# Performance work log

Measured on AMD Instinct MI355X. Metric: run time of the kernel, lower is better.

## Reference

```python
import jax, jax.numpy as jnp
import numpy as np

D_MODEL = 1024
N_HEADS = 16
B, T = 2, 2048


def setup_inputs() -> dict:
    key = jax.random.key(0)
    ks = jax.random.split(key, 5)
    scale = 1.0 / np.sqrt(D_MODEL)
    return {
        "x": jax.random.normal(ks[0], (B, T, D_MODEL), dtype=jnp.float32),
        "W_q": jax.random.normal(ks[1], (D_MODEL, D_MODEL), dtype=jnp.float32) * scale,
        "W_k": jax.random.normal(ks[2], (D_MODEL, D_MODEL), dtype=jnp.float32) * scale,
        "W_v": jax.random.normal(ks[3], (D_MODEL, D_MODEL), dtype=jnp.float32) * scale,
        "W_o": jax.random.normal(ks[4], (D_MODEL, D_MODEL), dtype=jnp.float32) * scale,
    }


def reference(x, W_q, W_k, W_v, W_o):
    Bn, Tn, D = x.shape
    H = N_HEADS
    Dh = D // H
    # nn.Linear(x) = x @ W.T ; weights stored as [out, in]
    q = (x @ W_q.T).reshape(Bn, Tn, H, Dh).transpose(0, 2, 1, 3)  # [B,H,T,Dh]
    k = (x @ W_k.T).reshape(Bn, Tn, H, Dh).transpose(0, 2, 1, 3)
    v = (x @ W_v.T).reshape(Bn, Tn, H, Dh).transpose(0, 2, 1, 3)
    scores = jnp.einsum("bhqd,bhkd->bhqk", q, k) / np.sqrt(Dh).astype(np.float32)
    attn = jax.nn.softmax(scores, axis=-1)  # [B,H,T,T]
    out = jnp.einsum("bhqk,bhkd->bhqd", attn, v)  # [B,H,T,Dh]
    out = out.transpose(0, 2, 1, 3).reshape(Bn, Tn, D)
    return out @ W_o.T
```

## Files before the change

kernel.cpp:

```cpp
#include <hip/hip_runtime.h>
#include <stdint.h>
#include <stddef.h>


typedef __bf16  bf16x8  __attribute__((ext_vector_type(8)));
typedef __bf16  bf16x4  __attribute__((ext_vector_type(4)));
typedef float   floatx4 __attribute__((ext_vector_type(4)));
typedef short   short4v __attribute__((ext_vector_type(4)));

#define DEV static __device__ __forceinline__

DEV void ld_g2l16(const void* g, void* l) {
    __builtin_amdgcn_global_load_lds(
        (__attribute__((address_space(1))) void*)g,
        (__attribute__((address_space(3))) void*)l,
        16, 0, 0);
}

DEV floatx4 mfma16(bf16x4 a, bf16x4 b, floatx4 c) {
#if defined(__HIP_DEVICE_COMPILE__)
    return __builtin_amdgcn_mfma_f32_16x16x16bf16_1k(
        __builtin_bit_cast(short4v, a), __builtin_bit_cast(short4v, b),
        c, 0, 0, 0);
#else
    (void)a; (void)b;
    return c;
#endif
}

#define WK_SCALE 0.18033688011112042f

__global__ __launch_bounds__(256) void cvt_all(
    const float* __restrict__ x,
    const float* __restrict__ wq, const float* __restrict__ wk,
    const float* __restrict__ wv, const float* __restrict__ wo,
    __bf16* __restrict__ xb,
    __bf16* __restrict__ wqb, __bf16* __restrict__ wkb,
    __bf16* __restrict__ wvb, __bf16* __restrict__ wob)
{
    unsigned u = blockIdx.x * 256u + threadIdx.x;
    const float* src;
    __bf16* dst;
    unsigned off;
    float mul = 1.0f;
    if (u < 1048576u) {
        src = x; dst = xb; off = u;
    } else {
        unsigned u2 = u - 1048576u;
        unsigned sel = u2 >> 18;
        off = u2 & 0x3FFFFu;
        src = (sel == 0) ? wq : (sel == 1) ? wk : (sel == 2) ? wv : wo;
        dst = (sel == 0) ? wqb : (sel == 1) ? wkb : (sel == 2) ? wvb : wob;
        if (sel == 1) mul = WK_SCALE;
    }
    float4 f = *(const float4*)(src + (size_t)off * 4);
    bf16x4 o = { (__bf16)(f.x * mul), (__bf16)(f.y * mul),
                 (__bf16)(f.z * mul), (__bf16)(f.w * mul) };
    *(bf16x4*)(dst + (size_t)off * 4) = o;
}

template<int BM, int NMAT, bool OUT_F32, bool TR_V>
__global__ __launch_bounds__(256) void gemm_bt(
    const __bf16* __restrict__ A,
    const __bf16* __restrict__ B0, const __bf16* __restrict__ B1,
    const __bf16* __restrict__ B2,
    void* __restrict__ C0, void* __restrict__ C1, void* __restrict__ C2)
{
    constexpr int Kd = 1024;
    constexpr int N  = 1024;
    constexpr int MI = BM / 32;
    constexpr int NA = BM / 64;
    __shared__ __bf16 As[BM * 32];
    __shared__ __bf16 Bs[128 * 32];

    const int t    = threadIdx.x;
    const int wid  = __builtin_amdgcn_readfirstlane(t >> 6);
    const int lane = t & 63;
    const int quad = lane >> 4;
    const int l15  = lane & 15;

    const int bx  = blockIdx.x;
    const int mat = (NMAT > 1) ? (bx >> 3) : 0;
    const int bn  = (NMAT > 1) ? (bx & 7)  : bx;
    const int bm  = blockIdx.y;
    const __bf16* Bm = (mat == 0) ? B0 : (mat == 1) ? B1 : B2;

    const __bf16* pA[NA];
    const __bf16* pB[2];
#pragma unroll
    for (int i = 0; i < NA; ++i) {
        int c    = i * 256 + t;
        int row  = c >> 2;
        int g    = (c & 3) ^ ((row >> 1) & 3);
        pA[i] = A + (size_t)(bm * BM + row) * Kd + g * 8;
    }
#pragma unroll
    for (int i = 0; i < 2; ++i) {
        int c    = i * 256 + t;
        int row  = c >> 2;
        int g    = (c & 3) ^ ((row >> 1) & 3);
        pB[i] = Bm + (size_t)(bn * 128 + row) * Kd + g * 8;
    }

    const int wm = wid >> 1;
    const int wn = wid & 1;
    const int slotr = quad ^ ((l15 >> 1) & 3);

    floatx4 acc[MI][4];
    const floatx4 z = { 0.f, 0.f, 0.f, 0.f };
#pragma unroll
    for (int i = 0; i < MI; ++i)
#pragma unroll
        for (int j = 0; j < 4; ++j) acc[i][j] = z;

    for (int kb = 0; kb < Kd; kb += 32) {
        __syncthreads();
#pragma unroll
        for (int i = 0; i < NA; ++i)
            ld_g2l16(pA[i] + kb, (char*)As + i * 4096 + wid * 1024);
#pragma unroll
        for (int i = 0; i < 2; ++i)
            ld_g2l16(pB[i] + kb, (char*)Bs + i * 4096 + wid * 1024);
        __syncthreads();

        bf16x8 af[MI], bf[4];
#pragma unroll
        for (int i = 0; i < MI; ++i) {
            int rowA = wm * (BM / 2) + i * 16 + l15;
            af[i] = *(const bf16x8*)&As[rowA * 32 + slotr * 8];
        }
#pragma unroll
        for (int j = 0; j < 4; ++j) {
            int rowB = wn * 64 + j * 16 + l15;
            bf[j] = *(const bf16x8*)&Bs[rowB * 32 + slotr * 8];
        }
#pragma unroll
        for (int i = 0; i < MI; ++i)
#pragma unroll
            for (int j = 0; j < 4; ++j)
                acc[i][j] = __builtin_amdgcn_mfma_f32_16x16x32_bf16(
                    af[i], bf[j], acc[i][j], 0, 0, 0);
    }

    const int row0 = bm * BM + wm * (BM / 2);
    const int col0 = bn * 128 + wn * 64;

    if (TR_V && mat == 2) {
        __bf16* Vt = (__bf16*)C2;
        const int bq    = bm >> 4;
        const int tloc0 = (row0 & 2047) + quad * 4;
#pragma unroll
        for (int i = 0; i < MI; ++i)
#pragma unroll
            for (int j = 0; j < 4; ++j) {
                int col = col0 + j * 16 + l15;
                int hh  = col >> 6, dh = col & 63;
                bf16x4 v = { (__bf16)acc[i][j][0], (__bf16)acc[i][j][1],
                             (__bf16)acc[i][j][2], (__bf16)acc[i][j][3] };
                *(bf16x4*)(Vt + ((size_t)(bq * 16 + hh) * 64 + dh) * 2048
                              + tloc0 + i * 16) = v;
            }
    } else {
        void* Cv = (mat == 0) ? C0 : (mat == 1) ? C1 : C2;
#pragma unroll
        for (int i = 0; i < MI; ++i)
#pragma unroll
            for (int j = 0; j < 4; ++j)
#pragma unroll
                for (int r = 0; r < 4; ++r) {
                    int grow = row0 + i * 16 + quad * 4 + r;
                    int gcol = col0 + j * 16 + l15;
                    if (OUT_F32)
                        ((float*)Cv)[(size_t)grow * N + gcol] = acc[i][j][r];
                    else
                        ((__bf16*)Cv)[(size_t)grow * N + gcol] =
                            (__bf16)acc[i][j][r];
                }
    }
}

__global__ __launch_bounds__(256, 2) void flash_kernel(
    const __bf16* __restrict__ Q, const __bf16* __restrict__ K,
    const __bf16* __restrict__ Vt, __bf16* __restrict__ O)
{
    __shared__ __bf16 Qs[128 * 64];
    __shared__ __bf16 Ks[2][64 * 64];
    __shared__ __bf16 Vs[2][64 * 64];

    const int t    = threadIdx.x;
    const int wid  = __builtin_amdgcn_readfirstlane(t >> 6);
    const int half = wid >> 1;
    const int wsub = wid & 1;
    const int lane = t & 63;
    const int quad = lane >> 4;
    const int l15  = lane & 15;
    const int qt   = blockIdx.x;
    const int bh   = blockIdx.y;
    const int b    = bh >> 4, h = bh & 15;

#pragma unroll
    for (int i = 0; i < 4; ++i) {
        int c = i * 256 + t;
        int row = c >> 3;
        int g   = (c & 7) ^ (row & 7);
        ld_g2l16(Q + (size_t)(b * 2048 + qt * 128 + row) * 1024 + h * 64 + g * 8,
                 (char*)Qs + i * 4096 + wid * 1024);
    }

    const __bf16* pK[2];
    const __bf16* pV[2];
#pragma unroll
    for (int i = 0; i < 2; ++i) {
        int c = i * 256 + t;
        int srow = c >> 3;
        int sg   = (c & 7) ^ (srow & 7);
        pK[i] = K  + (size_t)(b * 2048 + srow) * 1024 + h * 64 + sg * 8;
        pV[i] = Vt + (size_t)(bh * 64 + srow) * 2048 + sg * 8;
    }

    __syncthreads();

    bf16x8 qf[4][2];
#pragma unroll
    for (int nb = 0; nb < 4; ++nb)
#pragma unroll
        for (int ks = 0; ks < 2; ++ks) {
            int row  = wsub * 64 + nb * 16 + l15;
            int slot = (ks * 4 + quad) ^ (row & 7);
            qf[nb][ks] = *(const bf16x8*)&Qs[row * 64 + slot * 8];
        }

    int koff[2];
#pragma unroll
    for (int ks = 0; ks < 2; ++ks)
        koff[ks] = l15 * 128 + (((ks * 4 + quad) ^ (l15 & 7)) << 4);
    int voff[4];
#pragma unroll
    for (int k16 = 0; k16 < 4; ++k16)
        voff[k16] = l15 * 128 + (((k16 * 2 + (quad >> 1)) ^ (l15 & 7)) << 4)
                  + (quad & 1) * 8;

    const floatx4 z = { 0.f, 0.f, 0.f, 0.f };
    floatx4 o[4][4];
#pragma unroll
    for (int nb = 0; nb < 4; ++nb)
#pragma unroll
        for (int nd = 0; nd < 4; ++nd) o[nb][nd] = z;
    float lsum[4] = { 0.f, 0.f, 0.f, 0.f };

    for (int it = 0; it < 16; ++it) {
        __syncthreads();
#pragma unroll
        for (int i = 0; i < 2; ++i) {
            ld_g2l16(pK[i] + (size_t)it * 65536,
                     (char*)Ks[0] + i * 4096 + wid * 1024);
            ld_g2l16(pK[i] + (size_t)(16 + it) * 65536,
                     (char*)Ks[1] + i * 4096 + wid * 1024);
            ld_g2l16(pV[i] + it * 64,
                     (char*)Vs[0] + i * 4096 + wid * 1024);
            ld_g2l16(pV[i] + (16 + it) * 64,
                     (char*)Vs[1] + i * 4096 + wid * 1024);
        }
        __syncthreads();

        const char* kbase = (const char*)Ks[half];
        const char* vbase = (const char*)Vs[half];
#pragma unroll
        for (int kt16 = 0; kt16 < 4; ++kt16) {
            floatx4 s[4] = { z, z, z, z };
#pragma unroll
            for (int ks = 0; ks < 2; ++ks) {
                bf16x8 kf = *(const bf16x8*)(kbase + kt16 * 2048 + koff[ks]);
#pragma unroll
                for (int nb = 0; nb < 4; ++nb)
                    s[nb] = __builtin_amdgcn_mfma_f32_16x16x32_bf16(
                        kf, qf[nb][ks], s[nb], 0, 0, 0);
            }
            bf16x4 pb[4];
#pragma unroll
            for (int nb = 0; nb < 4; ++nb) {
                float p0 = __builtin_amdgcn_exp2f(s[nb][0]);
                float p1 = __builtin_amdgcn_exp2f(s[nb][1]);
                float p2 = __builtin_amdgcn_exp2f(s[nb][2]);
                float p3 = __builtin_amdgcn_exp2f(s[nb][3]);
                lsum[nb] += (p0 + p1) + (p2 + p3);
                bf16x4 pw = { (__bf16)p0, (__bf16)p1, (__bf16)p2, (__bf16)p3 };
                pb[nb] = pw;
            }
#pragma unroll
            for (int nd = 0; nd < 4; ++nd) {
                bf16x4 va = *(const bf16x4*)(vbase + nd * 2048 + voff[kt16]);
#pragma unroll
                for (int nb = 0; nb < 4; ++nb)
                    o[nb][nd] = mfma16(va, pb[nb], o[nb][nd]);
            }
        }
    }

    __syncthreads();
    float* obuf = (wsub == 0) ? (float*)&Ks[0][0] : (float*)&Vs[0][0];
    float* lbuf = (float*)&Qs[0] + wsub * 256;
    if (half == 1) {
#pragma unroll
        for (int nb = 0; nb < 4; ++nb)
#pragma unroll
            for (int nd = 0; nd < 4; ++nd)
                *(floatx4*)(obuf + (nb * 4 + nd) * 256 + lane * 4) = o[nb][nd];
#pragma unroll
        for (int nb = 0; nb < 4; ++nb) lbuf[nb * 64 + lane] = lsum[nb];
    }
    __syncthreads();
    if (half == 0) {
#pragma unroll
        for (int nb = 0; nb < 4; ++nb)
#pragma unroll
            for (int nd = 0; nd < 4; ++nd)
                o[nb][nd] += *(const floatx4*)(obuf + (nb * 4 + nd) * 256
                                               + lane * 4);
#pragma unroll
        for (int nb = 0; nb < 4; ++nb) {
            lsum[nb] += lbuf[nb * 64 + lane];
            lsum[nb] += __shfl_xor(lsum[nb], 16);
            lsum[nb] += __shfl_xor(lsum[nb], 32);
        }
#pragma unroll
        for (int nb = 0; nb < 4; ++nb) {
            float inv = 1.f / lsum[nb];
            int token = qt * 128 + wsub * 64 + nb * 16 + l15;
#pragma unroll
            for (int nd = 0; nd < 4; ++nd) {
                bf16x4 ov = { (__bf16)(o[nb][nd][0] * inv),
                              (__bf16)(o[nb][nd][1] * inv),
                              (__bf16)(o[nb][nd][2] * inv),
                              (__bf16)(o[nb][nd][3] * inv) };
                *(bf16x4*)(O + (size_t)(b * 2048 + token) * 1024
                             + h * 64 + nd * 16 + quad * 4) = ov;
            }
        }
    }
}

extern "C" void kernel_launch(void* const* d_in, const int* in_sizes, int n_in,
                              void* d_out, int out_size, void* d_ws, size_t ws_size,
                              hipStream_t stream)
{
    const float* x  = (const float*)d_in[0];
    const float* wq = (const float*)d_in[1];
    const float* wk = (const float*)d_in[2];
    const float* wv = (const float*)d_in[3];
    const float* wo = (const float*)d_in[4];

    char* ws = (char*)d_ws;
    __bf16* xb  = (__bf16*)(ws + 0);
    __bf16* wqb = (__bf16*)(ws + 8388608);
    __bf16* wkb = (__bf16*)(ws + 10485760);
    __bf16* wvb = (__bf16*)(ws + 12582912);
    __bf16* wob = (__bf16*)(ws + 14680064);
    __bf16* Qb  = (__bf16*)(ws + 16777216);
    __bf16* Kb  = (__bf16*)(ws + 25165824);
    __bf16* Vtb = (__bf16*)(ws + 33554432);
    __bf16* Ob  = xb;

    cvt_all<<<8192, 256, 0, stream>>>(x, wq, wk, wv, wo, xb, wqb, wkb, wvb, wob);

    gemm_bt<128, 3, false, true><<<dim3(24, 32), 256, 0, stream>>>(
        xb, wqb, wkb, wvb, (void*)Qb, (void*)Kb, (void*)Vtb);

    flash_kernel<<<dim3(16, 32), 256, 0, stream>>>(Qb, Kb, Vtb, Ob);

    gemm_bt<64, 1, true, false><<<dim3(8, 64), 256, 0, stream>>>(
        Ob, wob, nullptr, nullptr, d_out, nullptr, nullptr);
}
```

Before: 177.8 us.

## Split flash attention KV range across four wave pairs with 512-thread blocks

The flash kernel now runs 512 threads per block, and four wave pairs each process a quarter of the key/value sequence, where before two halves each covered half. Each iteration loads four KV tiles into LDS and the loop count halves. Partial outputs and row sums are merged through LDS in a two-level tree reduction. The aim is more waves per CU and fewer serial loop iterations per wave, at the cost of extra LDS (64KB total), more barriers in the reduction, and possible register pressure from the launch bounds of 512 threads with 4 blocks.

```diff
diff --git a/kernel.cpp b/kernel.cpp
--- a/kernel.cpp
+++ b/kernel.cpp
@@ -179,17 +179,17 @@
     }
 }
 
-__global__ __launch_bounds__(256, 2) void flash_kernel(
+__global__ __launch_bounds__(512, 4) void flash_kernel(
     const __bf16* __restrict__ Q, const __bf16* __restrict__ K,
     const __bf16* __restrict__ Vt, __bf16* __restrict__ O)
 {
     __shared__ __bf16 Qs[128 * 64];
-    __shared__ __bf16 Ks[2][64 * 64];
-    __shared__ __bf16 Vs[2][64 * 64];
+    __shared__ __bf16 Ks[4][64 * 64];
+    __shared__ __bf16 Vs[4][64 * 64];
 
     const int t    = threadIdx.x;
     const int wid  = __builtin_amdgcn_readfirstlane(t >> 6);
-    const int half = wid >> 1;
+    const int qtr  = wid >> 1;
     const int wsub = wid & 1;
     const int lane = t & 63;
     const int quad = lane >> 4;
@@ -199,24 +199,20 @@
     const int b    = bh >> 4, h = bh & 15;
 
 #pragma unroll
-    for (int i = 0; i < 4; ++i) {
-        int c = i * 256 + t;
+    for (int i = 0; i < 2; ++i) {
+        int c = i * 512 + t;
         int row = c >> 3;
         int g   = (c & 7) ^ (row & 7);
         ld_g2l16(Q + (size_t)(b * 2048 + qt * 128 + row) * 1024 + h * 64 + g * 8,
-                 (char*)Qs + i * 4096 + wid * 1024);
-    }
-
-    const __bf16* pK[2];
-    const __bf16* pV[2];
-#pragma unroll
-    for (int i = 0; i < 2; ++i) {
-        int c = i * 256 + t;
-        int srow = c >> 3;
-        int sg   = (c & 7) ^ (srow & 7);
-        pK[i] = K  + (size_t)(b * 2048 + srow) * 1024 + h * 64 + sg * 8;
-        pV[i] = Vt + (size_t)(bh * 64 + srow) * 2048 + sg * 8;
-    }
+                 (char*)Qs + i * 8192 + wid * 1024);
+    }
+
+    {
+    }
+    const int srow = t >> 3;
+    const int sg   = (t & 7) ^ (srow & 7);
+    const __bf16* pK = K  + (size_t)(b * 2048 + srow) * 1024 + h * 64 + sg * 8;
+    const __bf16* pV = Vt + (size_t)(bh * 64 + srow) * 2048 + sg * 8;
 
     __syncthreads();
 
@@ -248,23 +244,18 @@
         for (int nd = 0; nd < 4; ++nd) o[nb][nd] = z;
     float lsum[4] = { 0.f, 0.f, 0.f, 0.f };
 
-    for (int it = 0; it < 16; ++it) {
+    for (int it = 0; it < 8; ++it) {
         __syncthreads();
 #pragma unroll
-        for (int i = 0; i < 2; ++i) {
-            ld_g2l16(pK[i] + (size_t)it * 65536,
-                     (char*)Ks[0] + i * 4096 + wid * 1024);
-            ld_g2l16(pK[i] + (size_t)(16 + it) * 65536,
-                     (char*)Ks[1] + i * 4096 + wid * 1024);
-            ld_g2l16(pV[i] + it * 64,
-                     (char*)Vs[0] + i * 4096 + wid * 1024);
-            ld_g2l16(pV[i] + (16 + it) * 64,
-                     (char*)Vs[1] + i * 4096 + wid * 1024);
+        for (int qq = 0; qq < 4; ++qq) {
+            int kt = it * 4 + qq;
+            ld_g2l16(pK + (size_t)kt * 65536, (char*)Ks[qq] + wid * 1024);
+            ld_g2l16(pV + kt * 64,           (char*)Vs[qq] + wid * 1024);
         }
         __syncthreads();
 
-        const char* kbase = (const char*)Ks[half];
-        const char* vbase = (const char*)Vs[half];
+        const char* kbase = (const char*)Ks[qtr];
+        const char* vbase = (const char*)Vs[qtr];
 #pragma unroll
         for (int kt16 = 0; kt16 < 4; ++kt16) {
             floatx4 s[4] = { z, z, z, z };
@@ -297,29 +288,58 @@
         }
     }
 
-    __syncthreads();
-    float* obuf = (wsub == 0) ? (float*)&Ks[0][0] : (float*)&Vs[0][0];
-    float* lbuf = (float*)&Qs[0] + wsub * 256;
-    if (half == 1) {
+    float* obuf = (float*)&Ks[0][0];
+    float* lbuf = (float*)&Qs[0];
+    __syncthreads();
+    if (qtr >= 2) {
+        float* my = obuf + ((qtr - 2) * 2 + wsub) * 4096;
 #pragma unroll
         for (int nb = 0; nb < 4; ++nb)
 #pragma unroll
             for (int nd = 0; nd < 4; ++nd)
-                *(floatx4*)(obuf + (nb * 4 + nd) * 256 + lane * 4) = o[nb][nd];
-#pragma unroll
-        for (int nb = 0; nb < 4; ++nb) lbuf[nb * 64 + lane] = lsum[nb];
-    }
-    __syncthreads();
-    if (half == 0) {
+                *(floatx4*)(my + (nb * 4 + nd) * 256 + lane * 4) = o[nb][nd];
+        float* ml = lbuf + ((qtr - 2) * 2 + wsub) * 256;
+#pragma unroll
+        for (int nb = 0; nb < 4; ++nb) ml[nb * 64 + lane] = lsum[nb];
+    }
+    __syncthreads();
+    if (qtr < 2) {
+        float* pr = obuf + (qtr * 2 + wsub) * 4096;
 #pragma unroll
         for (int nb = 0; nb < 4; ++nb)
 #pragma unroll
             for (int nd = 0; nd < 4; ++nd)
-                o[nb][nd] += *(const floatx4*)(obuf + (nb * 4 + nd) * 256
+                o[nb][nd] += *(const floatx4*)(pr + (nb * 4 + nd) * 256
                                                + lane * 4);
+        float* pl = lbuf + (qtr * 2 + wsub) * 256;
+#pragma unroll
+        for (int nb = 0; nb < 4; ++nb) lsum[nb] += pl[nb * 64 + lane];
+    }
+    __syncthreads();
+    if (qtr == 1) {
+        float* my = obuf + wsub * 4096;
+#pragma unroll
+        for (int nb = 0; nb < 4; ++nb)
+#pragma unroll
+            for (int nd = 0; nd < 4; ++nd)
+                *(floatx4*)(my + (nb * 4 + nd) * 256 + lane * 4) = o[nb][nd];
+        float* ml = lbuf + wsub * 256;
+#pragma unroll
+        for (int nb = 0; nb < 4; ++nb) ml[nb * 64 + lane] = lsum[nb];
+    }
+    __syncthreads();
+    if (qtr == 0) {
+        float* pr = obuf + wsub * 4096;
+#pragma unroll
+        for (int nb = 0; nb < 4; ++nb)
+#pragma unroll
+            for (int nd = 0; nd < 4; ++nd)
+                o[nb][nd] += *(const floatx4*)(pr + (nb * 4 + nd) * 256
+                                               + lane * 4);
+        float* pl = lbuf + wsub * 256;
 #pragma unroll
         for (int nb = 0; nb < 4; ++nb) {
-            lsum[nb] += lbuf[nb * 64 + lane];
+            lsum[nb] += pl[nb * 64 + lane];
             lsum[nb] += __shfl_xor(lsum[nb], 16);
             lsum[nb] += __shfl_xor(lsum[nb], 32);
         }
@@ -366,7 +386,7 @@
     gemm_bt<128, 3, false, true><<<dim3(24, 32), 256, 0, stream>>>(
         xb, wqb, wkb, wvb, (void*)Qb, (void*)Kb, (void*)Vtb);
 
-    flash_kernel<<<dim3(16, 32), 256, 0, stream>>>(Qb, Kb, Vtb, Ob);
+    flash_kernel<<<dim3(16, 32), 512, 0, stream>>>(Qb, Kb, Vtb, Ob);
 
     gemm_bt<64, 1, true, false><<<dim3(8, 64), 256, 0, stream>>>(
         Ob, wob, nullptr, nullptr, d_out, nullptr, nullptr);
```

After: 453.1 us. 155% more time.
